# Kernel optimization log

Measured on AMD Instinct MI355X. Metric: run time of the kernel, lower is better.

Reference implementation:

```python
import jax, jax.numpy as jnp
import numpy as np

N = 50000      # entities
R = 400        # relations
D = 300        # init/hidden/output dim (hard-coded 300 in module)
E = 800000     # edges over N+R nodes
B = 2048       # aligned train pairs
L = 32         # padded neighbor sequence length
H, DK = 8, 32  # n_head=8, d_k=d_v=32
GAMMA1, GAMMA2 = 0.9, 0.2


def setup_inputs() -> dict:
    key = jax.random.key(0)
    ks = iter(jax.random.split(key, 48))
    nk = lambda: next(ks)
    inp = {}
    inp["e_x"] = jax.random.normal(nk(), (N, D), jnp.float32)
    inp["r_x"] = jax.random.normal(nk(), (R, 2 * D), jnp.float32)
    inp["edge_w"] = jax.random.uniform(nk(), (E,), jnp.float32)
    # learned params (fan-in scaled)
    s = lambda fi: 1.0 / np.sqrt(fi)
    inp["Wrel"] = jax.random.normal(nk(), (2 * D, D), jnp.float32) * s(2 * D)
    inp["brel"] = jnp.zeros((D,), jnp.float32)
    inp["W1"] = jax.random.normal(nk(), (D, D), jnp.float32) * s(D)
    inp["b1"] = jnp.zeros((D,), jnp.float32)
    inp["W2"] = jax.random.normal(nk(), (D, D), jnp.float32) * s(D)
    inp["b2"] = jnp.zeros((D,), jnp.float32)
    inp["Wprox"] = jax.random.normal(nk(), (2 * D, D), jnp.float32) * s(2 * D)
    inp["bprox"] = jnp.zeros((D,), jnp.float32)
    # encoder params, index 0 = input_encoder, 1 = output_encoder
    inp["enc_Wq"] = jax.random.normal(nk(), (2, D, H * DK), jnp.float32) * s(D)
    inp["enc_Wk"] = jax.random.normal(nk(), (2, D, H * DK), jnp.float32) * s(D)
    inp["enc_Wv"] = jax.random.normal(nk(), (2, D, H * DK), jnp.float32) * s(D)
    inp["enc_Wo"] = jax.random.normal(nk(), (2, H * DK, D), jnp.float32) * s(H * DK)
    # graph structure
    inp["edge_src"] = jax.random.randint(nk(), (E,), 0, N + R, jnp.int32)
    inp["edge_dst"] = jax.random.randint(nk(), (E,), 0, N + R, jnp.int32)
    # aligned entity pairs + padded neighbor (relation, head) sequences
    inp["l_ids"] = jax.random.randint(nk(), (B,), 0, N, jnp.int32)
    inp["r_ids"] = jax.random.randint(nk(), (B,), 0, N, jnp.int32)
    for p in ("l_in", "l_out", "r_in", "r_out"):
        inp[p + "_rel"] = jax.random.randint(nk(), (B, L), 0, R, jnp.int32)
        inp[p + "_head"] = jax.random.randint(nk(), (B, L), 0, N, jnp.int32)
        inp[p + "_mask"] = jax.random.randint(nk(), (B, L), 0, 2, jnp.int32).astype(bool)
    inp["train_len"] = B
    return inp


def _cosine(x, y):
    xn = x / jnp.maximum(jnp.linalg.norm(x, axis=1, keepdims=True), 1e-8)
    yn = y / jnp.maximum(jnp.linalg.norm(y, axis=1, keepdims=True), 1e-8)
    return xn @ yn.T


def _encoder(rel_seq, head_seq, mask, kernel, ent_f, rel_f, Wq, Wk, Wv, Wo):
    # neighbor tokens: relation emb + head entity emb    [B, L, D]
    tok = ent_f[head_seq] + rel_f[rel_seq]
    b = tok.shape[0]
    q = (kernel @ Wq).reshape(b, H, DK)                  # kernel entity is the query
    k = (tok @ Wk).reshape(b, L, H, DK)
    v = (tok @ Wv).reshape(b, L, H, DK)
    scores = jnp.einsum('bhd,blhd->bhl', q, k) / np.sqrt(DK)
    scores = jnp.where(mask[:, None, :], scores, -1e9)
    attn = jax.nn.softmax(scores, axis=-1)
    ctx = jnp.einsum('bhl,blhd->bhd', attn, v).reshape(b, H * DK)
    out = ctx @ Wo                                       # [B, D]
    # entities with empty neighbor list -> zero vector (original code path)
    return jnp.where(mask.any(-1)[:, None], out, 0.0)


def _get_proximity(ids, in_rel, in_head, in_mask, out_rel, out_head, out_mask,
                   ent_f, rel_f, enc_Wq, enc_Wk, enc_Wv, enc_Wo, Wprox, bprox):
    kernel = ent_f[ids]                                  # [B, D]
    in_em = _encoder(in_rel, in_head, in_mask, kernel, ent_f, rel_f,
                     enc_Wq[0], enc_Wk[0], enc_Wv[0], enc_Wo[0])
    out_em = _encoder(out_rel, out_head, out_mask, kernel, ent_f, rel_f,
                      enc_Wq[1], enc_Wk[1], enc_Wv[1], enc_Wo[1])
    prox = jnp.concatenate([in_em, out_em], axis=1) @ Wprox + bprox
    return jnp.concatenate([kernel, prox], axis=1)       # [B, 2D]


def reference(e_x, r_x, edge_w, Wrel, brel, W1, b1, W2, b2, Wprox, bprox,
              enc_Wq, enc_Wk, enc_Wv, enc_Wo,
              edge_src, edge_dst, l_ids, r_ids,
              l_in_rel, l_in_head, l_in_mask, l_out_rel, l_out_head, l_out_mask,
              r_in_rel, r_in_head, r_in_mask, r_out_rel, r_out_head, r_out_mask,
              train_len):
    NT = N + R
    # relation_linear then relational GCN over joint entity+relation graph
    r0 = r_x @ Wrel + brel                               # [R, D]
    x = jnp.concatenate([e_x, r0], axis=0)               # [NT, D]
    agg1 = jax.ops.segment_sum(edge_w[:, None] * x[edge_src], edge_dst, num_segments=NT)
    h1 = jax.nn.relu(agg1 @ W1 + b1)
    agg2 = jax.ops.segment_sum(edge_w[:, None] * h1[edge_src], edge_dst, num_segments=NT)
    h2 = agg2 @ W2 + b2
    gcn_ex, gcn_rx = h2[:N], h2[N:]
    # proximity embeddings for left/right aligned entities
    lem = _get_proximity(l_ids, l_in_rel, l_in_head, l_in_mask,
                         l_out_rel, l_out_head, l_out_mask,
                         gcn_ex, gcn_rx, enc_Wq, enc_Wk, enc_Wv, enc_Wo, Wprox, bprox)
    rem = _get_proximity(r_ids, r_in_rel, r_in_head, r_in_mask,
                         r_out_rel, r_out_head, r_out_mask,
                         gcn_ex, gcn_rx, enc_Wq, enc_Wk, enc_Wv, enc_Wo, Wprox, bprox)
    # contrastive alignment loss
    sim = _cosine(lem, rem)                              # [B, B]
    diag = jnp.diagonal(sim)
    pos_part = jnp.mean(jnp.minimum(diag, GAMMA1))
    no_diag = sim - jnp.diag(diag)
    neg_part = jnp.mean(jnp.maximum(no_diag, GAMMA2))
    loss = neg_part - GAMMA2 - pos_part + GAMMA1
    return loss, lem, rem
```

## Files before the change

kernel.cpp:

```cpp
#include <hip/hip_runtime.h>
#include <cstdint>
#include <cstddef>

typedef unsigned short u16;
typedef __attribute__((ext_vector_type(8))) short short8;
typedef __attribute__((ext_vector_type(4))) float f32x4;

#define NE 50000
#define NR 400
#define DD 300
#define NTOT 50400
#define EE 800000
#define BB 2048
#define LL 32
#define HD 256
#define KP1 320
#define KP2 608

__device__ inline void split2(float x, u16& hi, u16& lo) {
  unsigned u = __float_as_uint(x);
  unsigned hb = (u + 0x7fffu + ((u >> 16) & 1u)) >> 16;
  hi = (u16)hb;
  float hf = __uint_as_float(hb << 16);
  float l = x - hf;
  unsigned ul = __float_as_uint(l);
  lo = (u16)((ul + 0x7fffu + ((ul >> 16) & 1u)) >> 16);
}
__device__ inline float bf2f(u16 h) { return __uint_as_float(((unsigned)h) << 16); }

__global__ void copy_f4_kernel(const float4* __restrict__ src, float4* __restrict__ dst, int n4) {
  int i = blockIdx.x * blockDim.x + threadIdx.x;
  if (i < n4) dst[i] = src[i];
}

__global__ void rel_proj_kernel(const float* __restrict__ r_x, const float* __restrict__ Wrel,
                                const float* __restrict__ brel, float* __restrict__ out) {
  int row = blockIdx.x;
  int c = threadIdx.x;
  if (c >= DD) return;
  float acc = brel[c];
  const float* rr = r_x + (size_t)row * (2 * DD);
  for (int k = 0; k < 2 * DD; ++k) acc += rr[k] * Wrel[(size_t)k * DD + c];
  out[(size_t)row * DD + c] = acc;
}

__global__ void hist_kernel(const int* __restrict__ dst, int* __restrict__ counts) {
  int e = blockIdx.x * blockDim.x + threadIdx.x;
  if (e < EE) atomicAdd(&counts[dst[e]], 1);
}

__global__ __launch_bounds__(1024) void scan_kernel(const int* __restrict__ counts,
                                                    int* __restrict__ row_ptr,
                                                    int* __restrict__ cursor) {
  __shared__ int sums[1024];
  const int n = NTOT;
  int t = threadIdx.x;
  const int chunk = (n + 1023) / 1024;
  int begin = t * chunk;
  int end = begin + chunk; if (end > n) end = n;
  int s = 0;
  for (int i = begin; i < end; ++i) s += counts[i];
  sums[t] = s;
  __syncthreads();
  for (int off = 1; off < 1024; off <<= 1) {
    int v = (t >= off) ? sums[t - off] : 0;
    __syncthreads();
    sums[t] += v;
    __syncthreads();
  }
  int run = sums[t] - s;
  for (int i = begin; i < end; ++i) {
    row_ptr[i] = run; cursor[i] = run;
    run += counts[i];
  }
  if (t == 1023) row_ptr[n] = sums[1023];
}

__global__ void scatter_kernel(const int* __restrict__ dst, const int* __restrict__ src,
                               const float* __restrict__ w, int* __restrict__ cursor,
                               int* __restrict__ src_s, float* __restrict__ w_s) {
  int e = blockIdx.x * blockDim.x + threadIdx.x;
  if (e < EE) {
    int pos = atomicAdd(&cursor[dst[e]], 1);
    src_s[pos] = src[e];
    w_s[pos] = w[e];
  }
}

__global__ void detect_mask_kernel(const unsigned* __restrict__ m0, const unsigned* __restrict__ m1,
                                   const unsigned* __restrict__ m2, const unsigned* __restrict__ m3,
                                   int* __restrict__ flag) {
  int idx = blockIdx.x * blockDim.x + threadIdx.x;
  const int wp = BB * LL / 4;
  if (idx >= 4 * wp) return;
  const unsigned* p = idx < wp ? m0 : idx < 2 * wp ? m1 : idx < 3 * wp ? m2 : m3;
  if (p[idx % wp] > 1u) atomicOr(flag, 1);
}

__global__ void norm_mask_kernel(const void* __restrict__ raw, int* __restrict__ outm,
                                 int* __restrict__ many, const int* __restrict__ flag) {
  int idx = blockIdx.x * blockDim.x + threadIdx.x;
  if (idx >= BB * LL) return;
  int v = (*flag) ? (int)((const unsigned char*)raw)[idx] : ((const int*)raw)[idx];
  v = v ? 1 : 0;
  outm[idx] = v;
  if (v) atomicOr(&many[idx >> 5], 1);
}

__global__ __launch_bounds__(320) void aggregate_kernel(
    const float* __restrict__ feat, u16* __restrict__ outhi, u16* __restrict__ outlo,
    const int* __restrict__ row_ptr, const int* __restrict__ srcs, const float* __restrict__ ws) {
  int d = blockIdx.x;
  int f = threadIdx.x;
  if (f >= DD) return;
  int beg = row_ptr[d], end = row_ptr[d + 1];
  float acc = 0.f;
  int e = beg;
  for (; e + 8 <= end; e += 8) {
    int s[8]; float wv[8]; float v[8];
#pragma unroll
    for (int u = 0; u < 8; ++u) { s[u] = srcs[e + u]; wv[u] = ws[e + u]; }
#pragma unroll
    for (int u = 0; u < 8; ++u) v[u] = feat[(size_t)s[u] * DD + f];
#pragma unroll
    for (int u = 0; u < 8; ++u) acc += wv[u] * v[u];
  }
  for (; e + 2 <= end; e += 2) {
    int s0 = srcs[e], s1 = srcs[e + 1];
    float w0 = ws[e], w1 = ws[e + 1];
    acc += w0 * feat[(size_t)s0 * DD + f] + w1 * feat[(size_t)s1 * DD + f];
  }
  if (e < end) acc += ws[e] * feat[(size_t)srcs[e] * DD + f];
  u16 hi, lo; split2(acc, hi, lo);
  outhi[(size_t)d * KP1 + f] = hi;
  outlo[(size_t)d * KP1 + f] = lo;
}

__global__ void pad_zero_kernel(u16* __restrict__ hi, u16* __restrict__ lo, int rows, int ld, int c0) {
  int pw = ld - c0;
  int idx = blockIdx.x * blockDim.x + threadIdx.x;
  if (idx >= rows * pw) return;
  int r = idx / pw, c = c0 + idx % pw;
  hi[(size_t)r * ld + c] = 0;
  lo[(size_t)r * ld + c] = 0;
}

__global__ void transpose_split_kernel(const float* __restrict__ in, int insz,
                                       u16* __restrict__ outhi, u16* __restrict__ outlo, int outsz,
                                       int Kreal, int Nn, int Kpad) {
  int z = blockIdx.y;
  int idx = blockIdx.x * blockDim.x + threadIdx.x;
  if (idx >= Nn * Kpad) return;
  int n = idx / Kpad, k = idx % Kpad;
  float v = (k < Kreal) ? in[(size_t)z * insz + (size_t)k * Nn + n] : 0.f;
  u16 hi, lo; split2(v, hi, lo);
  outhi[(size_t)z * outsz + idx] = hi;
  outlo[(size_t)z * outsz + idx] = lo;
}

__global__ __launch_bounds__(256, 2) void mfma_gemm_kernel(
    const u16* __restrict__ Ahi, const u16* __restrict__ Alo, int lda,
    const u16* __restrict__ Bhi, const u16* __restrict__ Blo, int ldb,
    int M, int Nn, int K, const int* __restrict__ g1,
    float* __restrict__ C, int ldc, int coloff,
    const float* __restrict__ bias, int dorelu, const int* __restrict__ rowmask,
    u16* __restrict__ Chi, u16* __restrict__ Clo, int ldc16,
    int npass, int wofuse) {
  __shared__ int4 sAh[512], sAl[512], sBh[512], sBl[512];
  const int tid = threadIdx.x;
  const int row0 = blockIdx.y * 128, col0 = blockIdx.x * 128;
  const int wave = tid >> 6, lane = tid & 63;
  const int wrow = (wave >> 1) * 64, wcol = (wave & 1) * 64;
  const int m16 = lane & 15, quad = lane >> 4;

  const int sr = tid >> 2, sc = tid & 3;
  const u16* pah[2]; const u16* pal[2]; bool va[2];
  const u16* pbh[2]; const u16* pbl[2]; bool vb[2];
  int sidx[2];
#pragma unroll
  for (int i = 0; i < 2; ++i) {
    int r = sr + i * 64;
    sidx[i] = r * 4 + (sc ^ ((r >> 1) & 3));
    int grow = row0 + r;
    va[i] = grow < M;
    int ar = va[i] ? (g1 ? g1[grow] : grow) : 0;
    pah[i] = Ahi + (size_t)ar * lda + sc * 8;
    pal[i] = Alo + (size_t)ar * lda + sc * 8;
    int gn = col0 + r;
    vb[i] = gn < Nn;
    int br = vb[i] ? gn : 0;
    pbh[i] = Bhi + (size_t)br * ldb + sc * 8;
    pbl[i] = Blo + (size_t)br * ldb + sc * 8;
  }
  int idxA[4], idxB[4];
#pragma unroll
  for (int f = 0; f < 4; ++f) {
    int r = wrow + f * 16 + m16;
    idxA[f] = r * 4 + (quad ^ ((r >> 1) & 3));
    int n = wcol + f * 16 + m16;
    idxB[f] = n * 4 + (quad ^ ((n >> 1) & 3));
  }
  f32x4 acc[4][4];
#pragma unroll
  for (int i = 0; i < 4; ++i)
#pragma unroll
    for (int j = 0; j < 4; ++j) acc[i][j] = (f32x4){0.f, 0.f, 0.f, 0.f};

  const int4 z4 = {0, 0, 0, 0};
  for (int k0 = 0; k0 < K; k0 += 32) {
#pragma unroll
    for (int i = 0; i < 2; ++i) {
      int4 vh = z4, vl = z4, wh = z4, wl = z4;
      if (va[i]) { vh = *(const int4*)(pah[i] + k0); vl = *(const int4*)(pal[i] + k0); }
      if (vb[i]) { wh = *(const int4*)(pbh[i] + k0); wl = *(const int4*)(pbl[i] + k0); }
      sAh[sidx[i]] = vh; sAl[sidx[i]] = vl;
      sBh[sidx[i]] = wh; sBl[sidx[i]] = wl;
    }
    __syncthreads();
    short8 ah[4], al[4], bh[4], bl[4];
#pragma unroll
    for (int f = 0; f < 4; ++f) {
      ah[f] = *(const short8*)&sAh[idxA[f]];
      al[f] = *(const short8*)&sAl[idxA[f]];
      bh[f] = *(const short8*)&sBh[idxB[f]];
      bl[f] = *(const short8*)&sBl[idxB[f]];
    }
#pragma unroll
    for (int i = 0; i < 4; ++i)
#pragma unroll
      for (int j = 0; j < 4; ++j)
        acc[i][j] = __builtin_amdgcn_mfma_f32_16x16x32_bf16(ah[i], bh[j], acc[i][j], 0, 0, 0);
    if (npass > 1) {
#pragma unroll
      for (int i = 0; i < 4; ++i)
#pragma unroll
        for (int j = 0; j < 4; ++j)
          acc[i][j] = __builtin_amdgcn_mfma_f32_16x16x32_bf16(ah[i], bl[j], acc[i][j], 0, 0, 0);
#pragma unroll
      for (int i = 0; i < 4; ++i)
#pragma unroll
        for (int j = 0; j < 4; ++j)
          acc[i][j] = __builtin_amdgcn_mfma_f32_16x16x32_bf16(al[i], bh[j], acc[i][j], 0, 0, 0);
    }
    __syncthreads();
  }
#pragma unroll
  for (int i = 0; i < 4; ++i) {
#pragma unroll
    for (int reg = 0; reg < 4; ++reg) {
      int row = row0 + wrow + i * 16 + quad * 4 + reg;
      if (row >= M) continue;
      if (wofuse) {
        int b = row & 2047, side = (row >> 11) & 1, dir = (row >> 12) & 1;
        bool zero = rowmask[(side * 2 + dir) * BB + b] == 0;
        int orow = side * 2048 + b;
#pragma unroll
        for (int j = 0; j < 4; ++j) {
          int col = col0 + wcol + j * 16 + m16;
          if (col >= Nn) continue;
          if ((col >= 300) != (dir != 0)) continue;
          float v = acc[i][j][reg];
          if (zero) v = 0.f;
          u16 hb, lb; split2(v, hb, lb);
          Chi[(size_t)orow * ldc16 + col] = hb;
          Clo[(size_t)orow * ldc16 + col] = lb;
        }
        continue;
      }
      bool zero = (rowmask != nullptr) && (rowmask[row] == 0);
#pragma unroll
      for (int j = 0; j < 4; ++j) {
        int col = col0 + wcol + j * 16 + m16;
        if (col >= Nn) continue;
        float v = acc[i][j][reg];
        if (bias) v += bias[col];
        if (dorelu) v = fmaxf(v, 0.f);
        if (zero) v = 0.f;
        if (C) C[(size_t)row * ldc + coloff + col] = v;
        if (Chi) {
          u16 hb, lb; split2(v, hb, lb);
          Chi[(size_t)row * ldc16 + coloff + col] = hb;
          Clo[(size_t)row * ldc16 + coloff + col] = lb;
        }
      }
    }
  }
}

__global__ __launch_bounds__(256) void attention_kernel(
    const float* __restrict__ qb, const float* __restrict__ kv,
    const int* __restrict__ head_seq, const int* __restrict__ rel_seq,
    const int* __restrict__ masks, u16* __restrict__ ctxhi, u16* __restrict__ ctxlo) {
  int b = blockIdx.x;
  int tid = threadIdx.x;
  __shared__ float qs[256];
  __shared__ float attns[8][33];
  __shared__ int hid[32], rid[32], ms[32];
  qs[tid] = qb[(size_t)b * 512 + tid];
  if (tid < 32) {
    hid[tid] = head_seq[b * LL + tid];
    rid[tid] = NE + rel_seq[b * LL + tid];
    ms[tid] = masks[b * LL + tid];
  }
  __syncthreads();
  int h = tid >> 5, l = tid & 31;
  const float4* k1 = (const float4*)(kv + (size_t)hid[l] * 512 + h * 32);
  const float4* k2 = (const float4*)(kv + (size_t)rid[l] * 512 + h * 32);
  float s = 0.f;
#pragma unroll
  for (int i = 0; i < 8; ++i) {
    float4 a = k1[i], c4 = k2[i];
    const float* qp = &qs[h * 32 + i * 4];
    s += qp[0] * (a.x + c4.x) + qp[1] * (a.y + c4.y) + qp[2] * (a.z + c4.z) + qp[3] * (a.w + c4.w);
  }
  s *= 0.17677669529663687f;
  s = ms[l] ? s : -1e9f;
  float m = s;
  for (int off = 16; off; off >>= 1) m = fmaxf(m, __shfl_xor(m, off, 32));
  float e = expf(s - m);
  float sum = e;
  for (int off = 16; off; off >>= 1) sum += __shfl_xor(sum, off, 32);
  attns[h][l] = e / sum;
  __syncthreads();
  int d = tid & 31;
  float c = 0.f;
#pragma unroll 4
  for (int l2 = 0; l2 < 32; ++l2) {
    float a = attns[h][l2];
    float v = kv[(size_t)hid[l2] * 512 + 256 + h * 32 + d] +
              kv[(size_t)rid[l2] * 512 + 256 + h * 32 + d];
    c += a * v;
  }
  u16 hb, lb; split2(c, hb, lb);
  ctxhi[(size_t)b * 256 + tid] = hb;
  ctxlo[(size_t)b * 256 + tid] = lb;
}

__global__ void gather_part_kernel(const u16* __restrict__ enthi, const u16* __restrict__ entlo,
                                   const int* __restrict__ ids, float* __restrict__ out) {
  int b = blockIdx.x;
  int t = threadIdx.x;
  if (t < DD) {
    size_t o = (size_t)ids[b] * KP1 + t;
    out[(size_t)b * 600 + t] = bf2f(enthi[o]) + bf2f(entlo[o]);
  }
}

__global__ __launch_bounds__(256) void rownorm_kernel(const float* __restrict__ rows,
                                                      u16* __restrict__ outhi,
                                                      u16* __restrict__ outlo) {
  int b = blockIdx.x;
  int t = threadIdx.x;
  const float* rp = rows + (size_t)b * 600;
  float s = 0.f;
  for (int c = t; c < 600; c += 256) { float v = rp[c]; s += v * v; }
  __shared__ float red[256];
  red[t] = s;
  __syncthreads();
  for (int off = 128; off; off >>= 1) {
    if (t < off) red[t] += red[t + off];
    __syncthreads();
  }
  __shared__ float inv;
  if (t == 0) inv = 1.f / fmaxf(sqrtf(red[0]), 1e-8f);
  __syncthreads();
  for (int c = t; c < KP2; c += 256) {
    float v = (c < 600) ? rp[c] * inv : 0.f;
    u16 hb, lb; split2(v, hb, lb);
    outhi[(size_t)b * KP2 + c] = hb;
    outlo[(size_t)b * KP2 + c] = lb;
  }
}

__global__ __launch_bounds__(256) void loss_reduce_kernel(const float* __restrict__ sim,
                                                          double* __restrict__ accum) {
  __shared__ float rn_[256], rp_[256];
  float negs = 0.f, poss = 0.f;
  for (int idx = blockIdx.x * blockDim.x + threadIdx.x; idx < BB * BB;
       idx += gridDim.x * blockDim.x) {
    int i = idx >> 11, j = idx & (BB - 1);
    float s = sim[idx];
    if (i == j) {
      negs += 0.2f;
      poss += fminf(s, 0.9f);
    } else {
      negs += fmaxf(s, 0.2f);
    }
  }
  rn_[threadIdx.x] = negs; rp_[threadIdx.x] = poss;
  __syncthreads();
  for (int off = 128; off; off >>= 1) {
    if (threadIdx.x < off) {
      rn_[threadIdx.x] += rn_[threadIdx.x + off];
      rp_[threadIdx.x] += rp_[threadIdx.x + off];
    }
    __syncthreads();
  }
  if (threadIdx.x == 0) {
    atomicAdd(&accum[0], (double)rn_[0]);
    atomicAdd(&accum[1], (double)rp_[0]);
  }
}

__global__ void finalize_kernel(const double* __restrict__ accum, float* __restrict__ out) {
  double neg = accum[0] / ((double)BB * (double)BB);
  double pos = accum[1] / (double)BB;
  out[0] = (float)(neg - 0.2 - pos + 0.9);
}

static inline void launch_mfma(hipStream_t st, const u16* Ahi, const u16* Alo, int lda,
                               const u16* Bhi, const u16* Blo, int ldb, int M, int Nn, int K,
                               const int* g1, float* C, int ldc, int coloff, const float* bias,
                               int dorelu, const int* rowmask, u16* Chi, u16* Clo, int ldc16,
                               int npass = 3, int wofuse = 0) {
  dim3 grid((Nn + 127) / 128, (M + 127) / 128);
  mfma_gemm_kernel<<<grid, 256, 0, st>>>(Ahi, Alo, lda, Bhi, Blo, ldb, M, Nn, K, g1, C, ldc,
                                         coloff, bias, dorelu, rowmask, Chi, Clo, ldc16, npass,
                                         wofuse);
}

extern "C" void kernel_launch(void* const* d_in, const int* in_sizes, int n_in,
                              void* d_out, int out_size, void* d_ws, size_t ws_size,
                              hipStream_t stream) {
  const float* e_x    = (const float*)d_in[0];
  const float* r_x    = (const float*)d_in[1];
  const float* edge_w = (const float*)d_in[2];
  const float* Wrel   = (const float*)d_in[3];
  const float* brel   = (const float*)d_in[4];
  const float* W1     = (const float*)d_in[5];
  const float* b1     = (const float*)d_in[6];
  const float* W2     = (const float*)d_in[7];
  const float* b2     = (const float*)d_in[8];
  const float* Wprox  = (const float*)d_in[9];
  const float* bprox  = (const float*)d_in[10];
  const float* Wq     = (const float*)d_in[11];
  const float* Wk     = (const float*)d_in[12];
  const float* Wv     = (const float*)d_in[13];
  const float* Wo     = (const float*)d_in[14];
  const int* edge_src = (const int*)d_in[15];
  const int* edge_dst = (const int*)d_in[16];
  const int* l_ids    = (const int*)d_in[17];
  const int* r_ids    = (const int*)d_in[18];
  float* out = (float*)d_out;

  char* base = (char*)d_ws;
  size_t off = 0;
  auto nxt = [&](size_t bytes) -> char* {
    char* p = base + off;
    off += (bytes + 63) & ~(size_t)63;
    return p;
  };
  char* R0 = nxt(64512000);
  char* R1 = nxt(64512000);
  char* R2 = nxt(60480000);
  float* qbufL = (float*)nxt(4194304);
  float* qbufR = (float*)nxt(4194304);
  u16* ctxAhi = (u16*)nxt(4194304);
  u16* ctxAlo = (u16*)nxt(4194304);
  u16* emAhi  = (u16*)nxt(4980736);
  u16* emAlo  = (u16*)nxt(4980736);
  u16* lnhi   = (u16*)nxt(2490368);
  u16* lnlo   = (u16*)nxt(2490368);
  u16* rnhi   = (u16*)nxt(2490368);
  u16* rnlo   = (u16*)nxt(2490368);
  u16* qkvhi  = (u16*)nxt(983040);
  u16* qkvlo  = (u16*)nxt(983040);
  u16* w12hi  = (u16*)nxt(384000);
  u16* w12lo  = (u16*)nxt(384000);
  u16* wohi   = (u16*)nxt(307200);
  u16* wolo   = (u16*)nxt(307200);
  u16* wpxhi  = (u16*)nxt(364800);
  u16* wpxlo  = (u16*)nxt(364800);
  double* accum = (double*)nxt(16);
  int* row_ptr  = (int*)nxt(4 * (NTOT + 1));
  int* cursor   = (int*)nxt(4 * NTOT);
  int* counts   = (int*)nxt(4 * NTOT);
  int* src_s    = (int*)nxt(4 * EE);
  float* w_s    = (float*)nxt(4 * EE);
  int* mask_norm = (int*)nxt(4 * 4 * BB * LL);
  int* maskany   = (int*)nxt(4 * 4 * BB);
  int* flag      = (int*)nxt(64);

  float* xbuf = (float*)R0;
  u16* h2hi = (u16*)R0;  u16* h2lo = h2hi + (size_t)NTOT * KP1;
  u16* agghi = (u16*)R1; u16* agglo = agghi + (size_t)NTOT * KP1;
  float* kvbuf = (float*)R1;
  float* h1 = (float*)R2;
  float* simbuf = (float*)R1;

  hipMemsetAsync(counts, 0, NTOT * sizeof(int), stream);
  hipMemsetAsync(maskany, 0, 4 * BB * sizeof(int), stream);
  hipMemsetAsync(flag, 0, sizeof(int), stream);
  hipMemsetAsync(accum, 0, 2 * sizeof(double), stream);

  copy_f4_kernel<<<(3750000 + 255) / 256, 256, 0, stream>>>((const float4*)e_x, (float4*)xbuf,
                                                            3750000);
  rel_proj_kernel<<<NR, 320, 0, stream>>>(r_x, Wrel, brel, xbuf + (size_t)NE * DD);

  hist_kernel<<<(EE + 255) / 256, 256, 0, stream>>>(edge_dst, counts);
  scan_kernel<<<1, 1024, 0, stream>>>(counts, row_ptr, cursor);
  scatter_kernel<<<(EE + 255) / 256, 256, 0, stream>>>(edge_dst, edge_src, edge_w, cursor, src_s,
                                                       w_s);

  detect_mask_kernel<<<256, 256, 0, stream>>>((const unsigned*)d_in[21], (const unsigned*)d_in[24],
                                              (const unsigned*)d_in[27], (const unsigned*)d_in[30],
                                              flag);
  for (int mi = 0; mi < 4; ++mi)
    norm_mask_kernel<<<(BB * LL + 255) / 256, 256, 0, stream>>>(
        d_in[21 + mi * 3], mask_norm + (size_t)mi * BB * LL, maskany + mi * BB, flag);

  transpose_split_kernel<<<dim3((256 * KP1 + 255) / 256, 2), 256, 0, stream>>>(
      Wq, 300 * 256, qkvhi + 0 * 81920, qkvlo + 0 * 81920, 81920, 300, 256, KP1);
  transpose_split_kernel<<<dim3((256 * KP1 + 255) / 256, 1), 256, 0, stream>>>(
      Wk, 0, qkvhi + 2 * 81920, qkvlo + 2 * 81920, 81920, 300, 256, KP1);
  transpose_split_kernel<<<dim3((256 * KP1 + 255) / 256, 1), 256, 0, stream>>>(
      Wv, 0, qkvhi + 3 * 81920, qkvlo + 3 * 81920, 81920, 300, 256, KP1);
  transpose_split_kernel<<<dim3((256 * KP1 + 255) / 256, 1), 256, 0, stream>>>(
      Wk + 300 * 256, 0, qkvhi + 4 * 81920, qkvlo + 4 * 81920, 81920, 300, 256, KP1);
  transpose_split_kernel<<<dim3((256 * KP1 + 255) / 256, 1), 256, 0, stream>>>(
      Wv + 300 * 256, 0, qkvhi + 5 * 81920, qkvlo + 5 * 81920, 81920, 300, 256, KP1);
  transpose_split_kernel<<<dim3((300 * KP1 + 255) / 256, 1), 256, 0, stream>>>(
      W1, 0, w12hi, w12lo, 96000, 300, 300, KP1);
  transpose_split_kernel<<<dim3((300 * KP1 + 255) / 256, 1), 256, 0, stream>>>(
      W2, 0, w12hi + 96000, w12lo + 96000, 96000, 300, 300, KP1);
  transpose_split_kernel<<<dim3((300 * 256 + 255) / 256, 2), 256, 0, stream>>>(
      Wo, 256 * 300, wohi, wolo, 76800, 256, 300, 256);
  transpose_split_kernel<<<dim3((300 * KP2 + 255) / 256, 1), 256, 0, stream>>>(
      Wprox, 0, wpxhi, wpxlo, 182400, 600, 300, KP2);

  pad_zero_kernel<<<(NTOT * 20 + 255) / 256, 256, 0, stream>>>(agghi, agglo, NTOT, KP1, 300);
  pad_zero_kernel<<<(4096 * 8 + 255) / 256, 256, 0, stream>>>(emAhi, emAlo, 4096, KP2, 600);

  aggregate_kernel<<<NTOT, 320, 0, stream>>>(xbuf, agghi, agglo, row_ptr, src_s, w_s);
  launch_mfma(stream, agghi, agglo, KP1, w12hi, w12lo, KP1, NTOT, 300, KP1, nullptr, h1, 300, 0,
              b1, 1, nullptr, nullptr, nullptr, 0);
  aggregate_kernel<<<NTOT, 320, 0, stream>>>(h1, agghi, agglo, row_ptr, src_s, w_s);
  pad_zero_kernel<<<(NTOT * 20 + 255) / 256, 256, 0, stream>>>(h2hi, h2lo, NTOT, KP1, 300);
  launch_mfma(stream, agghi, agglo, KP1, w12hi + 96000, w12lo + 96000, KP1, NTOT, 300, KP1,
              nullptr, nullptr, 0, 0, b2, 0, nullptr, h2hi, h2lo, KP1);

  launch_mfma(stream, h2hi, h2lo, KP1, qkvhi, qkvlo, KP1, BB, 512, KP1, l_ids, qbufL, 512, 0,
              nullptr, 0, nullptr, nullptr, nullptr, 0);
  launch_mfma(stream, h2hi, h2lo, KP1, qkvhi, qkvlo, KP1, BB, 512, KP1, r_ids, qbufR, 512, 0,
              nullptr, 0, nullptr, nullptr, nullptr, 0);

  for (int dir = 0; dir < 2; ++dir) {
    launch_mfma(stream, h2hi, h2lo, KP1, qkvhi + (2 + 2 * dir) * 81920,
                qkvlo + (2 + 2 * dir) * 81920, KP1, NTOT, 512, KP1, nullptr, kvbuf, 512, 0,
                nullptr, 0, nullptr, nullptr, nullptr, 0);
    for (int side = 0; side < 2; ++side) {
      int mi = side * 2 + dir;
      const int* rel_seq  = (const int*)d_in[19 + side * 6 + dir * 3];
      const int* head_seq = (const int*)d_in[20 + side * 6 + dir * 3];
      const float* qb = (side ? qbufR : qbufL) + dir * 256;
      size_t cidx = (size_t)(dir * 2 + side) * BB * 256;
      attention_kernel<<<BB, 256, 0, stream>>>(qb, kvbuf, head_seq, rel_seq,
                                               mask_norm + (size_t)mi * BB * LL,
                                               ctxAhi + cidx, ctxAlo + cidx);
    }
  }

  launch_mfma(stream, ctxAhi, ctxAlo, 256, wohi, wolo, 256, 4 * BB, 600, 256, nullptr, nullptr,
              0, 0, nullptr, 0, maskany, emAhi, emAlo, KP2, 3, 1);

  float* lem = out + 1;
  float* rem = out + 1 + (size_t)BB * 600;
  launch_mfma(stream, emAhi, emAlo, KP2, wpxhi, wpxlo, KP2, 4096, 300, KP2, nullptr, lem, 600,
              300, bprox, 0, nullptr, nullptr, nullptr, 0);
  gather_part_kernel<<<BB, 320, 0, stream>>>(h2hi, h2lo, l_ids, lem);
  gather_part_kernel<<<BB, 320, 0, stream>>>(h2hi, h2lo, r_ids, rem);

  rownorm_kernel<<<BB, 256, 0, stream>>>(lem, lnhi, lnlo);
  rownorm_kernel<<<BB, 256, 0, stream>>>(rem, rnhi, rnlo);
  launch_mfma(stream, lnhi, lnlo, KP2, rnhi, rnlo, KP2, BB, BB, KP2, nullptr, simbuf, BB, 0,
              nullptr, 0, nullptr, nullptr, nullptr, 0, 1, 0);
  loss_reduce_kernel<<<2048, 256, 0, stream>>>(simbuf, accum);
  finalize_kernel<<<1, 1, 0, stream>>>(accum, out);
}
```

Before: 1.453 ms.

## Switch split-precision GEMMs to fp16, drop passes, fuse loss and batch launches

Replaces the bf16 hi/lo split with an fp16 hi/lo split and lets several GEMMs run with only two MFMA passes instead of three, skipping the low part of the B operand. This cuts matrix-core work and shared-memory loads for those GEMMs. The loss reduction is fused into the epilogue of the similarity GEMM, so the BxB sim matrix is never written or reread. The left and right Q projections are merged into one GEMM over concatenated ids, the attention launches are batched over sides, and the weight transpose now goes through a shared-memory tile. The risk is reduced accuracy from fp16 range and rounding and from the dropped correction pass, plus run-to-run variation from the atomic loss accumulation.

```diff
diff --git a/kernel.cpp b/kernel.cpp
--- a/kernel.cpp
+++ b/kernel.cpp
@@ -2,8 +2,8 @@
 #include <cstdint>
 #include <cstddef>
 
-typedef unsigned short u16;
-typedef __attribute__((ext_vector_type(8))) short short8;
+typedef _Float16 f16;
+typedef __attribute__((ext_vector_type(8))) _Float16 half8;
 typedef __attribute__((ext_vector_type(4))) float f32x4;
 
 #define NE 50000
@@ -17,16 +17,11 @@
 #define KP1 320
 #define KP2 608
 
-__device__ inline void split2(float x, u16& hi, u16& lo) {
-  unsigned u = __float_as_uint(x);
-  unsigned hb = (u + 0x7fffu + ((u >> 16) & 1u)) >> 16;
-  hi = (u16)hb;
-  float hf = __uint_as_float(hb << 16);
-  float l = x - hf;
-  unsigned ul = __float_as_uint(l);
-  lo = (u16)((ul + 0x7fffu + ((ul >> 16) & 1u)) >> 16);
-}
-__device__ inline float bf2f(u16 h) { return __uint_as_float(((unsigned)h) << 16); }
+__device__ inline void split2h(float x, f16& hi, f16& lo) {
+  f16 h = (f16)x;
+  hi = h;
+  lo = (f16)(x - (float)h);
+}
 
 __global__ void copy_f4_kernel(const float4* __restrict__ src, float4* __restrict__ dst, int n4) {
   int i = blockIdx.x * blockDim.x + threadIdx.x;
@@ -107,8 +102,15 @@
   if (v) atomicOr(&many[idx >> 5], 1);
 }
 
+__global__ void concat_ids_kernel(const int* __restrict__ a, const int* __restrict__ b,
+                                  int* __restrict__ o) {
+  int i = blockIdx.x * blockDim.x + threadIdx.x;
+  if (i < BB) o[i] = a[i];
+  else if (i < 2 * BB) o[i] = b[i - BB];
+}
+
 __global__ __launch_bounds__(320) void aggregate_kernel(
-    const float* __restrict__ feat, u16* __restrict__ outhi, u16* __restrict__ outlo,
+    const float* __restrict__ feat, f16* __restrict__ outhi, f16* __restrict__ outlo,
     const int* __restrict__ row_ptr, const int* __restrict__ srcs, const float* __restrict__ ws) {
   int d = blockIdx.x;
   int f = threadIdx.x;
@@ -131,41 +133,53 @@
     acc += w0 * feat[(size_t)s0 * DD + f] + w1 * feat[(size_t)s1 * DD + f];
   }
   if (e < end) acc += ws[e] * feat[(size_t)srcs[e] * DD + f];
-  u16 hi, lo; split2(acc, hi, lo);
+  f16 hi, lo; split2h(acc, hi, lo);
   outhi[(size_t)d * KP1 + f] = hi;
   outlo[(size_t)d * KP1 + f] = lo;
 }
 
-__global__ void pad_zero_kernel(u16* __restrict__ hi, u16* __restrict__ lo, int rows, int ld, int c0) {
+__global__ void pad_zero_kernel(f16* __restrict__ hi, f16* __restrict__ lo, int rows, int ld, int c0) {
   int pw = ld - c0;
   int idx = blockIdx.x * blockDim.x + threadIdx.x;
   if (idx >= rows * pw) return;
   int r = idx / pw, c = c0 + idx % pw;
-  hi[(size_t)r * ld + c] = 0;
-  lo[(size_t)r * ld + c] = 0;
-}
-
-__global__ void transpose_split_kernel(const float* __restrict__ in, int insz,
-                                       u16* __restrict__ outhi, u16* __restrict__ outlo, int outsz,
-                                       int Kreal, int Nn, int Kpad) {
-  int z = blockIdx.y;
-  int idx = blockIdx.x * blockDim.x + threadIdx.x;
-  if (idx >= Nn * Kpad) return;
-  int n = idx / Kpad, k = idx % Kpad;
-  float v = (k < Kreal) ? in[(size_t)z * insz + (size_t)k * Nn + n] : 0.f;
-  u16 hi, lo; split2(v, hi, lo);
-  outhi[(size_t)z * outsz + idx] = hi;
-  outlo[(size_t)z * outsz + idx] = lo;
+  hi[(size_t)r * ld + c] = (f16)0.f;
+  lo[(size_t)r * ld + c] = (f16)0.f;
+}
+
+__global__ __launch_bounds__(256) void transpose_split_kernel(
+    const float* __restrict__ in, int insz, f16* __restrict__ outhi, f16* __restrict__ outlo,
+    int outsz, int Kreal, int Nn, int Kpad) {
+  __shared__ float tile[32][33];
+  int z = blockIdx.z;
+  int k0 = blockIdx.x * 32, n0 = blockIdx.y * 32;
+  int tx = threadIdx.x & 31, ty = threadIdx.x >> 5;
+#pragma unroll
+  for (int r = 0; r < 4; ++r) {
+    int k = k0 + ty + r * 8, n = n0 + tx;
+    float v = (k < Kreal && n < Nn) ? in[(size_t)z * insz + (size_t)k * Nn + n] : 0.f;
+    tile[ty + r * 8][tx] = v;
+  }
+  __syncthreads();
+#pragma unroll
+  for (int r = 0; r < 4; ++r) {
+    int n = n0 + ty + r * 8, k = k0 + tx;
+    if (n < Nn && k < Kpad) {
+      f16 h, l; split2h(tile[tx][ty + r * 8], h, l);
+      outhi[(size_t)z * outsz + (size_t)n * Kpad + k] = h;
+      outlo[(size_t)z * outsz + (size_t)n * Kpad + k] = l;
+    }
+  }
 }
 
 __global__ __launch_bounds__(256, 2) void mfma_gemm_kernel(
-    const u16* __restrict__ Ahi, const u16* __restrict__ Alo, int lda,
-    const u16* __restrict__ Bhi, const u16* __restrict__ Blo, int ldb,
+    const f16* __restrict__ Ahi, const f16* __restrict__ Alo, int lda,
+    const f16* __restrict__ Bhi, const f16* __restrict__ Blo, int ldb,
     int M, int Nn, int K, const int* __restrict__ g1,
     float* __restrict__ C, int ldc, int coloff,
     const float* __restrict__ bias, int dorelu, const int* __restrict__ rowmask,
-    u16* __restrict__ Chi, u16* __restrict__ Clo, int ldc16,
-    int npass, int wofuse) {
+    f16* __restrict__ Chi, f16* __restrict__ Clo, int ldc16,
+    int npass, int wofuse, int losfuse, double* __restrict__ accum) {
   __shared__ int4 sAh[512], sAl[512], sBh[512], sBl[512];
   const int tid = threadIdx.x;
   const int row0 = blockIdx.y * 128, col0 = blockIdx.x * 128;
@@ -174,8 +188,8 @@
   const int m16 = lane & 15, quad = lane >> 4;
 
   const int sr = tid >> 2, sc = tid & 3;
-  const u16* pah[2]; const u16* pal[2]; bool va[2];
-  const u16* pbh[2]; const u16* pbl[2]; bool vb[2];
+  const f16* pah[2]; const f16* pal[2]; bool va[2];
+  const f16* pbh[2]; const f16* pbl[2]; bool vb[2];
   int sidx[2];
 #pragma unroll
   for (int i = 0; i < 2; ++i) {
@@ -210,40 +224,86 @@
   for (int k0 = 0; k0 < K; k0 += 32) {
 #pragma unroll
     for (int i = 0; i < 2; ++i) {
-      int4 vh = z4, vl = z4, wh = z4, wl = z4;
-      if (va[i]) { vh = *(const int4*)(pah[i] + k0); vl = *(const int4*)(pal[i] + k0); }
-      if (vb[i]) { wh = *(const int4*)(pbh[i] + k0); wl = *(const int4*)(pbl[i] + k0); }
-      sAh[sidx[i]] = vh; sAl[sidx[i]] = vl;
-      sBh[sidx[i]] = wh; sBl[sidx[i]] = wl;
+      int4 vh = z4, wh = z4;
+      if (va[i]) vh = *(const int4*)(pah[i] + k0);
+      if (vb[i]) wh = *(const int4*)(pbh[i] + k0);
+      sAh[sidx[i]] = vh; sBh[sidx[i]] = wh;
+      if (npass >= 2) {
+        int4 vl = z4;
+        if (va[i]) vl = *(const int4*)(pal[i] + k0);
+        sAl[sidx[i]] = vl;
+      }
+      if (npass >= 3) {
+        int4 wl = z4;
+        if (vb[i]) wl = *(const int4*)(pbl[i] + k0);
+        sBl[sidx[i]] = wl;
+      }
     }
     __syncthreads();
-    short8 ah[4], al[4], bh[4], bl[4];
+    half8 ah[4], bh[4];
 #pragma unroll
     for (int f = 0; f < 4; ++f) {
-      ah[f] = *(const short8*)&sAh[idxA[f]];
-      al[f] = *(const short8*)&sAl[idxA[f]];
-      bh[f] = *(const short8*)&sBh[idxB[f]];
-      bl[f] = *(const short8*)&sBl[idxB[f]];
+      ah[f] = *(const half8*)&sAh[idxA[f]];
+      bh[f] = *(const half8*)&sBh[idxB[f]];
     }
 #pragma unroll
     for (int i = 0; i < 4; ++i)
 #pragma unroll
       for (int j = 0; j < 4; ++j)
-        acc[i][j] = __builtin_amdgcn_mfma_f32_16x16x32_bf16(ah[i], bh[j], acc[i][j], 0, 0, 0);
-    if (npass > 1) {
+        acc[i][j] = __builtin_amdgcn_mfma_f32_16x16x32_f16(ah[i], bh[j], acc[i][j], 0, 0, 0);
+    if (npass >= 2) {
+      half8 al[4];
+#pragma unroll
+      for (int f = 0; f < 4; ++f) al[f] = *(const half8*)&sAl[idxA[f]];
 #pragma unroll
       for (int i = 0; i < 4; ++i)
 #pragma unroll
         for (int j = 0; j < 4; ++j)
-          acc[i][j] = __builtin_amdgcn_mfma_f32_16x16x32_bf16(ah[i], bl[j], acc[i][j], 0, 0, 0);
+          acc[i][j] = __builtin_amdgcn_mfma_f32_16x16x32_f16(al[i], bh[j], acc[i][j], 0, 0, 0);
+    }
+    if (npass >= 3) {
+      half8 bl[4];
+#pragma unroll
+      for (int f = 0; f < 4; ++f) bl[f] = *(const half8*)&sBl[idxB[f]];
 #pragma unroll
       for (int i = 0; i < 4; ++i)
 #pragma unroll
         for (int j = 0; j < 4; ++j)
-          acc[i][j] = __builtin_amdgcn_mfma_f32_16x16x32_bf16(al[i], bh[j], acc[i][j], 0, 0, 0);
+          acc[i][j] = __builtin_amdgcn_mfma_f32_16x16x32_f16(ah[i], bl[j], acc[i][j], 0, 0, 0);
     }
     __syncthreads();
   }
+
+  if (losfuse) {
+    float negs = 0.f, poss = 0.f;
+#pragma unroll
+    for (int i = 0; i < 4; ++i)
+#pragma unroll
+      for (int reg = 0; reg < 4; ++reg) {
+        int row = row0 + wrow + i * 16 + quad * 4 + reg;
+#pragma unroll
+        for (int j = 0; j < 4; ++j) {
+          int col = col0 + wcol + j * 16 + m16;
+          float s = acc[i][j][reg];
+          if (row == col) { negs += 0.2f; poss += fminf(s, 0.9f); }
+          else negs += fmaxf(s, 0.2f);
+        }
+      }
+    float* rn_ = (float*)sAh;
+    float* rp_ = (float*)sAl;
+    rn_[tid] = negs; rp_[tid] = poss;
+    __syncthreads();
+    for (int off2 = 128; off2; off2 >>= 1) {
+      if (tid < off2) { rn_[tid] += rn_[tid + off2]; rp_[tid] += rp_[tid + off2]; }
+      __syncthreads();
+    }
+    if (tid == 0) {
+      atomicAdd(&accum[0], (double)rn_[0]);
+      atomicAdd(&accum[1], (double)rp_[0]);
+    }
+    return;
+  }
+
 #pragma unroll
   for (int i = 0; i < 4; ++i) {
 #pragma unroll
@@ -261,7 +321,7 @@
           if ((col >= 300) != (dir != 0)) continue;
           float v = acc[i][j][reg];
           if (zero) v = 0.f;
-          u16 hb, lb; split2(v, hb, lb);
+          f16 hb, lb; split2h(v, hb, lb);
           Chi[(size_t)orow * ldc16 + col] = hb;
           Clo[(size_t)orow * ldc16 + col] = lb;
         }
@@ -278,7 +338,7 @@
         if (zero) v = 0.f;
         if (C) C[(size_t)row * ldc + coloff + col] = v;
         if (Chi) {
-          u16 hb, lb; split2(v, hb, lb);
+          f16 hb, lb; split2h(v, hb, lb);
           Chi[(size_t)row * ldc16 + coloff + col] = hb;
           Clo[(size_t)row * ldc16 + coloff + col] = lb;
         }
@@ -288,19 +348,24 @@
 }
 
 __global__ __launch_bounds__(256) void attention_kernel(
-    const float* __restrict__ qb, const float* __restrict__ kv,
-    const int* __restrict__ head_seq, const int* __restrict__ rel_seq,
-    const int* __restrict__ masks, u16* __restrict__ ctxhi, u16* __restrict__ ctxlo) {
+    const float* __restrict__ qAll, const float* __restrict__ kv,
+    const int* __restrict__ h0, const int* __restrict__ r0, const int* __restrict__ m0,
+    const int* __restrict__ h1, const int* __restrict__ r1, const int* __restrict__ m1,
+    int dirOfs, f16* __restrict__ ctxhi, f16* __restrict__ ctxlo) {
   int b = blockIdx.x;
+  int side = blockIdx.y;
   int tid = threadIdx.x;
+  const int* hs = side ? h1 : h0;
+  const int* rs = side ? r1 : r0;
+  const int* msk = side ? m1 : m0;
   __shared__ float qs[256];
   __shared__ float attns[8][33];
   __shared__ int hid[32], rid[32], ms[32];
-  qs[tid] = qb[(size_t)b * 512 + tid];
+  qs[tid] = qAll[((size_t)(side * BB + b)) * 512 + dirOfs + tid];
   if (tid < 32) {
-    hid[tid] = head_seq[b * LL + tid];
-    rid[tid] = NE + rel_seq[b * LL + tid];
-    ms[tid] = masks[b * LL + tid];
+    hid[tid] = hs[b * LL + tid];
+    rid[tid] = NE + rs[b * LL + tid];
+    ms[tid] = msk[b * LL + tid];
   }
   __syncthreads();
   int h = tid >> 5, l = tid & 31;
@@ -331,24 +396,25 @@
               kv[(size_t)rid[l2] * 512 + 256 + h * 32 + d];
     c += a * v;
   }
-  u16 hb, lb; split2(c, hb, lb);
-  ctxhi[(size_t)b * 256 + tid] = hb;
-  ctxlo[(size_t)b * 256 + tid] = lb;
-}
-
-__global__ void gather_part_kernel(const u16* __restrict__ enthi, const u16* __restrict__ entlo,
+  f16 hb, lb; split2h(c, hb, lb);
+  size_t o = ((size_t)side * BB + b) * 256 + tid;
+  ctxhi[o] = hb;
+  ctxlo[o] = lb;
+}
+
+__global__ void gather_part_kernel(const f16* __restrict__ enthi, const f16* __restrict__ entlo,
                                    const int* __restrict__ ids, float* __restrict__ out) {
   int b = blockIdx.x;
   int t = threadIdx.x;
   if (t < DD) {
     size_t o = (size_t)ids[b] * KP1 + t;
-    out[(size_t)b * 600 + t] = bf2f(enthi[o]) + bf2f(entlo[o]);
+    out[(size_t)b * 600 + t] = (float)enthi[o] + (float)entlo[o];
   }
 }
 
 __global__ __launch_bounds__(256) void rownorm_kernel(const float* __restrict__ rows,
-                                                      u16* __restrict__ outhi,
-                                                      u16* __restrict__ outlo) {
+                                                      f16* __restrict__ outhi,
+                                                      f16* __restrict__ outlo) {
   int b = blockIdx.x;
   int t = threadIdx.x;
   const float* rp = rows + (size_t)b * 600;
@@ -366,39 +432,9 @@
   __syncthreads();
   for (int c = t; c < KP2; c += 256) {
     float v = (c < 600) ? rp[c] * inv : 0.f;
-    u16 hb, lb; split2(v, hb, lb);
+    f16 hb, lb; split2h(v, hb, lb);
     outhi[(size_t)b * KP2 + c] = hb;
     outlo[(size_t)b * KP2 + c] = lb;
-  }
-}
-
-__global__ __launch_bounds__(256) void loss_reduce_kernel(const float* __restrict__ sim,
-                                                          double* __restrict__ accum) {
-  __shared__ float rn_[256], rp_[256];
-  float negs = 0.f, poss = 0.f;
-  for (int idx = blockIdx.x * blockDim.x + threadIdx.x; idx < BB * BB;
-       idx += gridDim.x * blockDim.x) {
-    int i = idx >> 11, j = idx & (BB - 1);
-    float s = sim[idx];
-    if (i == j) {
-      negs += 0.2f;
-      poss += fminf(s, 0.9f);
-    } else {
-      negs += fmaxf(s, 0.2f);
-    }
-  }
-  rn_[threadIdx.x] = negs; rp_[threadIdx.x] = poss;
-  __syncthreads();
-  for (int off = 128; off; off >>= 1) {
-    if (threadIdx.x < off) {
-      rn_[threadIdx.x] += rn_[threadIdx.x + off];
-      rp_[threadIdx.x] += rp_[threadIdx.x + off];
-    }
-    __syncthreads();
-  }
-  if (threadIdx.x == 0) {
-    atomicAdd(&accum[0], (double)rn_[0]);
-    atomicAdd(&accum[1], (double)rp_[0]);
   }
 }
 
@@ -408,15 +444,22 @@
   out[0] = (float)(neg - 0.2 - pos + 0.9);
 }
 
-static inline void launch_mfma(hipStream_t st, const u16* Ahi, const u16* Alo, int lda,
-                               const u16* Bhi, const u16* Blo, int ldb, int M, int Nn, int K,
+static inline void launch_mfma(hipStream_t st, const f16* Ahi, const f16* Alo, int lda,
+                               const f16* Bhi, const f16* Blo, int ldb, int M, int Nn, int K,
                                const int* g1, float* C, int ldc, int coloff, const float* bias,
-                               int dorelu, const int* rowmask, u16* Chi, u16* Clo, int ldc16,
-                               int npass = 3, int wofuse = 0) {
+                               int dorelu, const int* rowmask, f16* Chi, f16* Clo, int ldc16,
+                               int npass = 3, int wofuse = 0, int losfuse = 0,
+                               double* accum = nullptr) {
   dim3 grid((Nn + 127) / 128, (M + 127) / 128);
   mfma_gemm_kernel<<<grid, 256, 0, st>>>(Ahi, Alo, lda, Bhi, Blo, ldb, M, Nn, K, g1, C, ldc,
                                          coloff, bias, dorelu, rowmask, Chi, Clo, ldc16, npass,
-                                         wofuse);
+                                         wofuse, losfuse, accum);
+}
+
+static inline void launch_transpose(hipStream_t st, const float* in, int insz, f16* oh, f16* ol,
+                                    int outsz, int Kreal, int Nn, int Kpad, int z) {
+  dim3 grid((Kpad + 31) / 32, (Nn + 31) / 32, z);
+  transpose_split_kernel<<<grid, 256, 0, st>>>(in, insz, oh, ol, outsz, Kreal, Nn, Kpad);
 }
 
 extern "C" void kernel_launch(void* const* d_in, const int* in_sizes, int n_in,
@@ -453,24 +496,23 @@
   char* R0 = nxt(64512000);
   char* R1 = nxt(64512000);
   char* R2 = nxt(60480000);
-  float* qbufL = (float*)nxt(4194304);
-  float* qbufR = (float*)nxt(4194304);
-  u16* ctxAhi = (u16*)nxt(4194304);
-  u16* ctxAlo = (u16*)nxt(4194304);
-  u16* emAhi  = (u16*)nxt(4980736);
-  u16* emAlo  = (u16*)nxt(4980736);
-  u16* lnhi   = (u16*)nxt(2490368);
-  u16* lnlo   = (u16*)nxt(2490368);
-  u16* rnhi   = (u16*)nxt(2490368);
-  u16* rnlo   = (u16*)nxt(2490368);
-  u16* qkvhi  = (u16*)nxt(983040);
-  u16* qkvlo  = (u16*)nxt(983040);
-  u16* w12hi  = (u16*)nxt(384000);
-  u16* w12lo  = (u16*)nxt(384000);
-  u16* wohi   = (u16*)nxt(307200);
-  u16* wolo   = (u16*)nxt(307200);
-  u16* wpxhi  = (u16*)nxt(364800);
-  u16* wpxlo  = (u16*)nxt(364800);
+  float* qAll  = (float*)nxt(8388608);
+  f16* ctxAhi = (f16*)nxt(4194304);
+  f16* ctxAlo = (f16*)nxt(4194304);
+  f16* emAhi  = (f16*)nxt(4980736);
+  f16* emAlo  = (f16*)nxt(4980736);
+  f16* lnhi   = (f16*)nxt(2490368);
+  f16* lnlo   = (f16*)nxt(2490368);
+  f16* rnhi   = (f16*)nxt(2490368);
+  f16* rnlo   = (f16*)nxt(2490368);
+  f16* qkvhi  = (f16*)nxt(983040);
+  f16* qkvlo  = (f16*)nxt(983040);
+  f16* w12hi  = (f16*)nxt(384000);
+  f16* w12lo  = (f16*)nxt(384000);
+  f16* wohi   = (f16*)nxt(307200);
+  f16* wolo   = (f16*)nxt(307200);
+  f16* wpxhi  = (f16*)nxt(364800);
+  f16* wpxlo  = (f16*)nxt(364800);
   double* accum = (double*)nxt(16);
   int* row_ptr  = (int*)nxt(4 * (NTOT + 1));
   int* cursor   = (int*)nxt(4 * NTOT);
@@ -479,14 +521,14 @@
   float* w_s    = (float*)nxt(4 * EE);
   int* mask_norm = (int*)nxt(4 * 4 * BB * LL);
   int* maskany   = (int*)nxt(4 * 4 * BB);
+  int* idsAll    = (int*)nxt(4 * 2 * BB);
   int* flag      = (int*)nxt(64);
 
   float* xbuf = (float*)R0;
-  u16* h2hi = (u16*)R0;  u16* h2lo = h2hi + (size_t)NTOT * KP1;
-  u16* agghi = (u16*)R1; u16* agglo = agghi + (size_t)NTOT * KP1;
+  f16* h2hi = (f16*)R0;  f16* h2lo = h2hi + (size_t)NTOT * KP1;
+  f16* agghi = (f16*)R1; f16* agglo = agghi + (size_t)NTOT * KP1;
   float* kvbuf = (float*)R1;
   float* h1 = (float*)R2;
-  float* simbuf = (float*)R1;
 
   hipMemsetAsync(counts, 0, NTOT * sizeof(int), stream);
   hipMemsetAsync(maskany, 0, 4 * BB * sizeof(int), stream);
@@ -508,56 +550,46 @@
   for (int mi = 0; mi < 4; ++mi)
     norm_mask_kernel<<<(BB * LL + 255) / 256, 256, 0, stream>>>(
         d_in[21 + mi * 3], mask_norm + (size_t)mi * BB * LL, maskany + mi * BB, flag);
-
-  transpose_split_kernel<<<dim3((256 * KP1 + 255) / 256, 2), 256, 0, stream>>>(
-      Wq, 300 * 256, qkvhi + 0 * 81920, qkvlo + 0 * 81920, 81920, 300, 256, KP1);
-  transpose_split_kernel<<<dim3((256 * KP1 + 255) / 256, 1), 256, 0, stream>>>(
-      Wk, 0, qkvhi + 2 * 81920, qkvlo + 2 * 81920, 81920, 300, 256, KP1);
-  transpose_split_kernel<<<dim3((256 * KP1 + 255) / 256, 1), 256, 0, stream>>>(
-      Wv, 0, qkvhi + 3 * 81920, qkvlo + 3 * 81920, 81920, 300, 256, KP1);
-  transpose_split_kernel<<<dim3((256 * KP1 + 255) / 256, 1), 256, 0, stream>>>(
-      Wk + 300 * 256, 0, qkvhi + 4 * 81920, qkvlo + 4 * 81920, 81920, 300, 256, KP1);
-  transpose_split_kernel<<<dim3((256 * KP1 + 255) / 256, 1), 256, 0, stream>>>(
-      Wv + 300 * 256, 0, qkvhi + 5 * 81920, qkvlo + 5 * 81920, 81920, 300, 256, KP1);
-  transpose_split_kernel<<<dim3((300 * KP1 + 255) / 256, 1), 256, 0, stream>>>(
-      W1, 0, w12hi, w12lo, 96000, 300, 300, KP1);
-  transpose_split_kernel<<<dim3((300 * KP1 + 255) / 256, 1), 256, 0, stream>>>(
-      W2, 0, w12hi + 96000, w12lo + 96000, 96000, 300, 300, KP1);
-  transpose_split_kernel<<<dim3((300 * 256 + 255) / 256, 2), 256, 0, stream>>>(
-      Wo, 256 * 300, wohi, wolo, 76800, 256, 300, 256);
-  transpose_split_kernel<<<dim3((300 * KP2 + 255) / 256, 1), 256, 0, stream>>>(
-      Wprox, 0, wpxhi, wpxlo, 182400, 600, 300, KP2);
+  concat_ids_kernel<<<(2 * BB + 255) / 256, 256, 0, stream>>>(l_ids, r_ids, idsAll);
+
+  launch_transpose(stream, Wq, 300 * 256, qkvhi + 0 * 81920, qkvlo + 0 * 81920, 81920, 300, 256,
+                   KP1, 2);
+  launch_transpose(stream, Wk, 0, qkvhi + 2 * 81920, qkvlo + 2 * 81920, 81920, 300, 256, KP1, 1);
+  launch_transpose(stream, Wv, 0, qkvhi + 3 * 81920, qkvlo + 3 * 81920, 81920, 300, 256, KP1, 1);
+  launch_transpose(stream, Wk + 300 * 256, 0, qkvhi + 4 * 81920, qkvlo + 4 * 81920, 81920, 300,
+                   256, KP1, 1);
+  launch_transpose(stream, Wv + 300 * 256, 0, qkvhi + 5 * 81920, qkvlo + 5 * 81920, 81920, 300,
+                   256, KP1, 1);
+  launch_transpose(stream, W1, 0, w12hi, w12lo, 96000, 300, 300, KP1, 1);
+  launch_transpose(stream, W2, 0, w12hi + 96000, w12lo + 96000, 96000, 300, 300, KP1, 1);
+  launch_transpose(stream, Wo, 256 * 300, wohi, wolo, 76800, 256, 300, 256, 2);
+  launch_transpose(stream, Wprox, 0, wpxhi, wpxlo, 182400, 600, 300, KP2, 1);
 
   pad_zero_kernel<<<(NTOT * 20 + 255) / 256, 256, 0, stream>>>(agghi, agglo, NTOT, KP1, 300);
   pad_zero_kernel<<<(4096 * 8 + 255) / 256, 256, 0, stream>>>(emAhi, emAlo, 4096, KP2, 600);
 
   aggregate_kernel<<<NTOT, 320, 0, stream>>>(xbuf, agghi, agglo, row_ptr, src_s, w_s);
   launch_mfma(stream, agghi, agglo, KP1, w12hi, w12lo, KP1, NTOT, 300, KP1, nullptr, h1, 300, 0,
-              b1, 1, nullptr, nullptr, nullptr, 0);
+              b1, 1, nullptr, nullptr, nullptr, 0, 2);
   aggregate_kernel<<<NTOT, 320, 0, stream>>>(h1, agghi, agglo, row_ptr, src_s, w_s);
   pad_zero_kernel<<<(NTOT * 20 + 255) / 256, 256, 0, stream>>>(h2hi, h2lo, NTOT, KP1, 300);
   launch_mfma(stream, agghi, agglo, KP1, w12hi + 96000, w12lo + 96000, KP1, NTOT, 300, KP1,
-              nullptr, nullptr, 0, 0, b2, 0, nullptr, h2hi, h2lo, KP1);
-
-  launch_mfma(stream, h2hi, h2lo, KP1, qkvhi, qkvlo, KP1, BB, 512, KP1, l_ids, qbufL, 512, 0,
-              nullptr, 0, nullptr, nullptr, nullptr, 0);
-  launch_mfma(stream, h2hi, h2lo, KP1, qkvhi, qkvlo, KP1, BB, 512, KP1, r_ids, qbufR, 512, 0,
-              nullptr, 0, nullptr, nullptr, nullptr, 0);
+              nullptr, nullptr, 0, 0, b2, 0, nullptr, h2hi, h2lo, KP1, 3);
+
+  launch_mfma(stream, h2hi, h2lo, KP1, qkvhi, qkvlo, KP1, 2 * BB, 512, KP1, idsAll, qAll, 512, 0,
+              nullptr, 0, nullptr, nullptr, nullptr, 0, 2);
 
   for (int dir = 0; dir < 2; ++dir) {
     launch_mfma(stream, h2hi, h2lo, KP1, qkvhi + (2 + 2 * dir) * 81920,
                 qkvlo + (2 + 2 * dir) * 81920, KP1, NTOT, 512, KP1, nullptr, kvbuf, 512, 0,
-                nullptr, 0, nullptr, nullptr, nullptr, 0);
-    for (int side = 0; side < 2; ++side) {
-      int mi = side * 2 + dir;
-      const int* rel_seq  = (const int*)d_in[19 + side * 6 + dir * 3];
-      const int* head_seq = (const int*)d_in[20 + side * 6 + dir * 3];
-      const float* qb = (side ? qbufR : qbufL) + dir * 256;
-      size_t cidx = (size_t)(dir * 2 + side) * BB * 256;
-      attention_kernel<<<BB, 256, 0, stream>>>(qb, kvbuf, head_seq, rel_seq,
-                                               mask_norm + (size_t)mi * BB * LL,
-                                               ctxAhi + cidx, ctxAlo + cidx);
-    }
+                nullptr, 0, nullptr, nullptr, nullptr, 0, 2);
+    attention_kernel<<<dim3(BB, 2), 256, 0, stream>>>(
+        qAll, kvbuf,
+        (const int*)d_in[20 + dir * 3], (const int*)d_in[19 + dir * 3],
+        mask_norm + (size_t)(0 * 2 + dir) * BB * LL,
+        (const int*)d_in[26 + dir * 3], (const int*)d_in[25 + dir * 3],
+        mask_norm + (size_t)(1 * 2 + dir) * BB * LL,
+        dir * 256, ctxAhi + (size_t)dir * 2 * BB * 256, ctxAlo + (size_t)dir * 2 * BB * 256);
   }
 
   launch_mfma(stream, ctxAhi, ctxAlo, 256, wohi, wolo, 256, 4 * BB, 600, 256, nullptr, nullptr,
@@ -566,14 +598,13 @@
   float* lem = out + 1;
   float* rem = out + 1 + (size_t)BB * 600;
   launch_mfma(stream, emAhi, emAlo, KP2, wpxhi, wpxlo, KP2, 4096, 300, KP2, nullptr, lem, 600,
-              300, bprox, 0, nullptr, nullptr, nullptr, 0);
+              300, bprox, 0, nullptr, nullptr, nullptr, 0, 3);
   gather_part_kernel<<<BB, 320, 0, stream>>>(h2hi, h2lo, l_ids, lem);
   gather_part_kernel<<<BB, 320, 0, stream>>>(h2hi, h2lo, r_ids, rem);
 
   rownorm_kernel<<<BB, 256, 0, stream>>>(lem, lnhi, lnlo);
   rownorm_kernel<<<BB, 256, 0, stream>>>(rem, rnhi, rnlo);
-  launch_mfma(stream, lnhi, lnlo, KP2, rnhi, rnlo, KP2, BB, BB, KP2, nullptr, simbuf, BB, 0,
-              nullptr, 0, nullptr, nullptr, nullptr, 0, 1, 0);
-  loss_reduce_kernel<<<2048, 256, 0, stream>>>(simbuf, accum);
+  launch_mfma(stream, lnhi, lnlo, KP2, rnhi, rnlo, KP2, BB, BB, KP2, nullptr, nullptr, 0, 0,
+              nullptr, 0, nullptr, nullptr, nullptr, 0, 1, 0, 1, accum);
   finalize_kernel<<<1, 1, 0, stream>>>(accum, out);
 }
```

New measurement: 1.409 ms. -3.0%, faster.
